# Kernel tuning notes

Hardware: AMD Instinct MI355X
Metric: run time of the kernel (lower is better)

The kernel has to match this reference:

```python
import jax, jax.numpy as jnp
import numpy as np

DIM = 1024
NE = 4            # num_experts
MLP = 4           # mlp_ratio
H = 16            # num_heads
HD = DIM // H     # head dim
EXP = 3 * DIM + MLP * DIM   # expand output dim (7*dim)
CIN = DIM + MLP * DIM       # contract input dim (5*dim)


def layer_norm(x, g, b, eps=1e-5):
    m = jnp.mean(x, axis=-1, keepdims=True)
    v = jnp.var(x, axis=-1, keepdims=True)
    return (x - m) * jax.lax.rsqrt(v + eps) * g + b


def setup_inputs() -> dict:
    key = jax.random.key(0)
    ks = jax.random.split(key, 8)
    B, N = 8, 1024
    x = jax.random.normal(ks[0], (B, N, DIM), jnp.float32)
    expert_mask = jax.random.randint(ks[1], (B, N), 0, NE, jnp.int32)
    router_probs = jax.random.uniform(ks[2], (B, N, NE), jnp.float32)
    expand_weight = jax.random.normal(ks[3], (EXP, DIM), jnp.float32) * 0.02
    mlp_bias = jnp.zeros((MLP * DIM,), jnp.float32)
    contract_weight = jax.random.normal(ks[4], (2 * DIM, CIN), jnp.float32) * 0.02
    contract_bias = jnp.zeros((2 * DIM,), jnp.float32)
    norm1_g = jnp.ones((DIM,), jnp.float32)
    norm1_b = jnp.zeros((DIM,), jnp.float32)
    norm2_g = jnp.ones((DIM,), jnp.float32)
    norm2_b = jnp.zeros((DIM,), jnp.float32)
    alpha = jnp.zeros((1,), jnp.float32)
    return dict(x=x, expert_mask=expert_mask, router_probs=router_probs,
                expand_weight=expand_weight, mlp_bias=mlp_bias,
                contract_weight=contract_weight, contract_bias=contract_bias,
                norm1_g=norm1_g, norm1_b=norm1_b, norm2_g=norm2_g, norm2_b=norm2_b,
                alpha=alpha)


def reference(x, expert_mask, router_probs, expand_weight, mlp_bias,
              contract_weight, contract_bias, norm1_g, norm1_b,
              norm2_g, norm2_b, alpha):
    B, N, _ = x.shape
    shift = (NE - 1 - expert_mask).astype(jnp.int32)          # [B,N]
    # nested (matryoshka) active dims per token
    d_in = DIM // jnp.left_shift(1, shift)                    # expand: active input dims
    d_out = (2 * DIM) // jnp.left_shift(1, shift)             # contract: active output dims

    # nested_linear_expand: zero inactive input features, then full GEMM
    in_mask = (jnp.arange(DIM) < d_in[..., None]).astype(x.dtype)
    xn = layer_norm(x, norm1_g, norm1_b) * in_mask
    y = jnp.einsum('bnd,od->bno', xn, expand_weight)          # [B,N,7*dim]

    qkv = y[..., :3 * DIM]
    mlp_hidden = y[..., 3 * DIM:] + mlp_bias

    q = qkv[..., :DIM]
    k = layer_norm(qkv[..., DIM:2 * DIM], norm2_g, norm2_b)
    v = layer_norm(qkv[..., 2 * DIM:], norm2_g, norm2_b)

    qh = q.reshape(B, N, H, HD)
    kh = k.reshape(B, N, H, HD)
    vh = v.reshape(B, N, H, HD)
    scale = HD ** -0.5
    attn = jax.nn.softmax(jnp.einsum('bqhd,bkhd->bhqk', qh, kh) * scale, axis=-1)
    attn_out = jnp.einsum('bhqk,bkhd->bqhd', attn, vh).reshape(B, N, DIM)

    h = jnp.concatenate([attn_out, jax.nn.gelu(mlp_hidden, approximate=False)], axis=-1)
    # nested_linear_contract: full GEMM, zero inactive output features
    z = jnp.einsum('bnc,oc->bno', h, contract_weight) + contract_bias  # [B,N,2*dim]
    z = z * (jnp.arange(2 * DIM) < d_out[..., None]).astype(z.dtype)

    attn_o = z[..., :DIM] + x
    mlp_o = z[..., DIM:]
    expert_probs = jnp.take_along_axis(router_probs, expert_mask[..., None].astype(jnp.int32), axis=-1)  # [B,N,1]
    out = attn_o + (alpha * expert_probs + 1.0) * mlp_o
    return (out, expert_mask, router_probs)
```

## Files before the change

kernel.cpp:

```cpp
#include <hip/hip_runtime.h>
#include <hip/hip_bf16.h>
#include <math.h>

typedef __bf16 bf16_t;
typedef __attribute__((ext_vector_type(8))) __bf16 bf16x8;
typedef __attribute__((ext_vector_type(4))) __bf16 bf16x4;
typedef __attribute__((ext_vector_type(4))) float f32x4;
typedef __attribute__((ext_vector_type(4))) unsigned u32x4;

typedef __attribute__((address_space(1))) unsigned as1u;
typedef __attribute__((address_space(3))) unsigned as3u;

#define MAXT1 68
#define MAXJ2 2112

__device__ __forceinline__ void async_copy16(bf16_t* lds, const bf16_t* g) {
  __builtin_amdgcn_global_load_lds((as1u*)g, (as3u*)lds, 16, 0, 0);
}

__device__ __forceinline__ float gelu_exact(float t) {
  return 0.5f * t * (1.0f + erff(t * 0.70710678118654752f));
}

__device__ __forceinline__ unsigned pack_bf16(float a, float b) {
  unsigned short ha = __builtin_bit_cast(unsigned short, (bf16_t)a);
  unsigned short hb = __builtin_bit_cast(unsigned short, (bf16_t)b);
  return (unsigned)ha | ((unsigned)hb << 16);
}

__global__ __launch_bounds__(256)
void cast_kernel(const float* __restrict__ w, bf16_t* __restrict__ o, int n) {
  int i = (blockIdx.x * 256 + threadIdx.x) * 4;
  if (i < n) {
    float4 v = *(const float4*)(w + i);
    bf16x4 t;
    t[0] = (bf16_t)v.x; t[1] = (bf16_t)v.y; t[2] = (bf16_t)v.z; t[3] = (bf16_t)v.w;
    *(bf16x4*)(o + i) = t;
  }
}

__global__ __launch_bounds__(1024)
void sort_kernel(const int* __restrict__ em, int* __restrict__ perm,
                 int* __restrict__ t1, int* __restrict__ j2) {
  __shared__ int cnt[4], cur[4], tb[5], jb[5];
  const int tid = threadIdx.x;
  const int wave = tid >> 6, lane = tid & 63;
  if (tid < 4) cnt[tid] = 0;
  __syncthreads();
  for (int c = wave; c < 128; c += 16) {
    int e = em[c * 64 + lane];
    unsigned long long m0 = __ballot(e == 0), m1 = __ballot(e == 1);
    unsigned long long m2 = __ballot(e == 2), m3 = __ballot(e == 3);
    if (lane == 0) {
      atomicAdd(&cnt[0], (int)__popcll(m0)); atomicAdd(&cnt[1], (int)__popcll(m1));
      atomicAdd(&cnt[2], (int)__popcll(m2)); atomicAdd(&cnt[3], (int)__popcll(m3));
    }
  }
  __syncthreads();
  if (tid == 0) {
    cur[0] = 0; cur[1] = cnt[0]; cur[2] = cnt[0] + cnt[1]; cur[3] = cnt[0] + cnt[1] + cnt[2];
    tb[0] = 0; jb[0] = 0;
    for (int i = 0; i < 4; ++i) {
      int e = 3 - i;
      tb[i + 1] = tb[i] + ((cnt[e] + 127) >> 7);
    }
    for (int e = 0; e < 4; ++e) {
      int nt = (cnt[e] + 127) >> 7;
      jb[e + 1] = jb[e] + nt * (4 << e);
    }
  }
  __syncthreads();
  for (int c = wave; c < 128; c += 16) {
    int i = c * 64 + lane;
    int e = em[i];
    unsigned long long m0 = __ballot(e == 0), m1 = __ballot(e == 1);
    unsigned long long m2 = __ballot(e == 2), m3 = __ballot(e == 3);
    unsigned long long me = e == 0 ? m0 : e == 1 ? m1 : e == 2 ? m2 : m3;
    int bl = 0;
    if (lane < 4) {
      unsigned long long ml = lane == 0 ? m0 : lane == 1 ? m1 : lane == 2 ? m2 : m3;
      bl = atomicAdd(&cur[lane], (int)__popcll(ml));
    }
    int base = __shfl(bl, e);
    unsigned long long lt = (1ull << lane) - 1ull;
    perm[base + (int)__popcll(me & lt)] = i;
  }
  int offp[5];
  offp[0] = 0;
  #pragma unroll
  for (int e = 0; e < 4; ++e) offp[e + 1] = offp[e] + cnt[e];
  for (int t = tid; t < MAXT1; t += 1024) {
    int e = -1, loc = 0;
    #pragma unroll
    for (int i = 0; i < 4; ++i) if (t >= tb[i] && t < tb[i + 1]) { e = 3 - i; loc = t - tb[i]; }
    if (e >= 0) {
      t1[t * 3] = e; t1[t * 3 + 1] = offp[e] + loc * 128;
      t1[t * 3 + 2] = min(128, cnt[e] - loc * 128);
    } else t1[t * 3] = -1;
  }
  for (int j = tid; j < MAXJ2; j += 1024) {
    int e = -1, loc = 0;
    #pragma unroll
    for (int q = 0; q < 4; ++q) if (j >= jb[q] && j < jb[q + 1]) { e = q; loc = j - jb[q]; }
    if (e >= 0) {
      int t = loc >> (2 + e), b = loc & ((4 << e) - 1);
      j2[j * 4] = e; j2[j * 4 + 1] = offp[e] + t * 128;
      j2[j * 4 + 2] = min(128, cnt[e] - t * 128); j2[j * 4 + 3] = b;
    } else j2[j * 4] = -1;
  }
}

__global__ __launch_bounds__(256)
void ln1_kernel(const float* __restrict__ x, const float* __restrict__ gam,
                const float* __restrict__ bet, const int* __restrict__ em,
                bf16_t* __restrict__ xn) {
  const int row = blockIdx.x, tid = threadIdx.x;
  const float4 v = ((const float4*)(x + (size_t)row * 1024))[tid];
  float s = v.x + v.y + v.z + v.w;
  float sq = v.x * v.x + v.y * v.y + v.z * v.z + v.w * v.w;
  #pragma unroll
  for (int off = 1; off < 64; off <<= 1) { s += __shfl_xor(s, off); sq += __shfl_xor(sq, off); }
  __shared__ float red[8];
  const int wave = tid >> 6, lane = tid & 63;
  if (lane == 0) { red[wave] = s; red[4 + wave] = sq; }
  __syncthreads();
  s = red[0] + red[1] + red[2] + red[3];
  sq = red[4] + red[5] + red[6] + red[7];
  const float mean = s * (1.0f / 1024.0f);
  const float var = sq * (1.0f / 1024.0f) - mean * mean;
  const float rstd = rsqrtf(var + 1e-5f);
  const int din = 1024 >> (3 - em[row]);
  const float4 gv = ((const float4*)gam)[tid];
  const float4 bv = ((const float4*)bet)[tid];
  const int c0 = tid * 4;
  float vf[4] = {v.x, v.y, v.z, v.w};
  float gf[4] = {gv.x, gv.y, gv.z, gv.w};
  float bvf[4] = {bv.x, bv.y, bv.z, bv.w};
  bf16x4 o;
  #pragma unroll
  for (int i = 0; i < 4; ++i) {
    float t = (vf[i] - mean) * rstd * gf[i] + bvf[i];
    o[i] = (c0 + i < din) ? (bf16_t)t : (bf16_t)0.0f;
  }
  *(bf16x4*)(xn + (size_t)row * 1024 + c0) = o;
}

__global__ __launch_bounds__(256)
void ln2_kernel(bf16_t* __restrict__ kv, const float* __restrict__ gam,
                const float* __restrict__ bet) {
  const int row = blockIdx.x, tid = threadIdx.x;
  bf16_t* base = kv + (size_t)row * 2048;
  bf16x4 kk = *(const bf16x4*)(base + tid * 4);
  bf16x4 vv = *(const bf16x4*)(base + 1024 + tid * 4);
  float kf[4], vf[4];
  float ks = 0, ksq = 0, vs = 0, vsq = 0;
  #pragma unroll
  for (int i = 0; i < 4; ++i) {
    kf[i] = (float)kk[i]; ks += kf[i]; ksq += kf[i] * kf[i];
    vf[i] = (float)vv[i]; vs += vf[i]; vsq += vf[i] * vf[i];
  }
  #pragma unroll
  for (int off = 1; off < 64; off <<= 1) {
    ks += __shfl_xor(ks, off); ksq += __shfl_xor(ksq, off);
    vs += __shfl_xor(vs, off); vsq += __shfl_xor(vsq, off);
  }
  __shared__ float red[16];
  const int wave = tid >> 6, lane = tid & 63;
  if (lane == 0) { red[wave] = ks; red[4 + wave] = ksq; red[8 + wave] = vs; red[12 + wave] = vsq; }
  __syncthreads();
  ks = red[0] + red[1] + red[2] + red[3];
  ksq = red[4] + red[5] + red[6] + red[7];
  vs = red[8] + red[9] + red[10] + red[11];
  vsq = red[12] + red[13] + red[14] + red[15];
  const float mk = ks * (1.f / 1024.f), mv = vs * (1.f / 1024.f);
  const float rk = rsqrtf(ksq * (1.f / 1024.f) - mk * mk + 1e-5f);
  const float rv = rsqrtf(vsq * (1.f / 1024.f) - mv * mv + 1e-5f);
  const float4 gv = ((const float4*)gam)[tid];
  const float4 bv = ((const float4*)bet)[tid];
  float gf[4] = {gv.x, gv.y, gv.z, gv.w}, bvf[4] = {bv.x, bv.y, bv.z, bv.w};
  bf16x4 ko, vo;
  #pragma unroll
  for (int i = 0; i < 4; ++i) {
    ko[i] = (bf16_t)((kf[i] - mk) * rk * gf[i] + bvf[i]);
    vo[i] = (bf16_t)((vf[i] - mv) * rv * gf[i] + bvf[i]);
  }
  *(bf16x4*)(base + tid * 4) = ko;
  *(bf16x4*)(base + 1024 + tid * 4) = vo;
}

__global__ __launch_bounds__(256)
void vt_kernel(const bf16_t* __restrict__ kv, bf16_t* __restrict__ vT) {
  __shared__ bf16_t t[64][80];
  const int tt = blockIdx.x, head = blockIdx.y;
  const int tid = threadIdx.x;
  const int r8 = tid >> 3, c8 = tid & 7;
  #pragma unroll
  for (int i = 0; i < 2; ++i) {
    const int tok = i * 32 + r8;
    bf16x8 v = *(const bf16x8*)(kv + (size_t)(tt * 64 + tok) * 2048 + 1024 + head * 64 + c8 * 8);
    #pragma unroll
    for (int j = 0; j < 8; ++j) t[c8 * 8 + j][tok] = v[j];
  }
  __syncthreads();
  const int bb = tt >> 4;
  const int tloc = (tt & 15) * 64;
  #pragma unroll
  for (int i = 0; i < 2; ++i) {
    const int d = i * 32 + r8;
    bf16x8 v = *(const bf16x8*)(&t[d][c8 * 8]);
    *(bf16x8*)(vT + (size_t)((bb * 16 + head) * 64 + d) * 1024 + tloc + c8 * 8) = v;
  }
}

template<int EPI>
__global__ __launch_bounds__(256)
void gemm_bt(const bf16_t* __restrict__ A, const bf16_t* __restrict__ W,
             const int* __restrict__ perm, const int* __restrict__ desc,
             const float* __restrict__ bias,
             bf16_t* __restrict__ hb, bf16_t* __restrict__ kvb,
             bf16_t* __restrict__ z) {
  constexpr int K = (EPI == 0) ? 1024 : 5120;
  constexpr int BN = (EPI == 0) ? 128 : 64;
  constexpr int NI = BN / 32;
  constexpr int WC = BN / 2;
  const int* d = desc + ((EPI == 0) ? blockIdx.y * 3 : blockIdx.x * 4);
  const int e = d[0];
  if (e < 0) return;
  const int nval = d[2];
  const int bn = (EPI == 0) ? blockIdx.x : d[3];
  const int nkt = (EPI == 0) ? (2 << e) : 80;

  __shared__ bf16_t SMEM[17408];
  __shared__ int prow[128];
  bf16_t* As = SMEM;
  bf16_t* Bs = SMEM + 8192;

  const int tid = threadIdx.x;
  if (tid < 128) prow[tid] = perm[d[1] + min(tid, nval - 1)];
  const int wave = tid >> 6, lane = tid & 63;
  const int l15 = lane & 15, l4 = lane >> 4;
  const int wm = wave >> 1, wn = wave & 1;

  f32x4 acc[4][NI] = {};

  const int rbase = tid >> 3;
  const int ss = (tid & 7) ^ (rbase & 7);
  __syncthreads();
  const bf16_t* Ag[4];
  #pragma unroll
  for (int i = 0; i < 4; ++i) Ag[i] = A + (size_t)prow[i * 32 + rbase] * K + ss * 8;
  const bf16_t* Wg = W + (size_t)(bn * BN + rbase) * K + ss * 8;

  for (int kt = 0; kt < nkt; ++kt) {
    #pragma unroll
    for (int i = 0; i < 4; ++i)
      async_copy16(As + (i * 256 + wave * 64) * 8, Ag[i] + kt * 64);
    #pragma unroll
    for (int i = 0; i < NI; ++i)
      async_copy16(Bs + (i * 256 + wave * 64) * 8, Wg + (size_t)(i * 32) * K + kt * 64);
    __syncthreads();
    #pragma unroll
    for (int ks = 0; ks < 2; ++ks) {
      bf16x8 a[4], b[NI];
      #pragma unroll
      for (int mi = 0; mi < 4; ++mi) {
        const int r = wm * 64 + mi * 16 + l15;
        const int slot = (ks * 4 + l4) ^ (r & 7);
        a[mi] = *(const bf16x8*)(As + r * 64 + slot * 8);
      }
      #pragma unroll
      for (int ni = 0; ni < NI; ++ni) {
        const int r = wn * WC + ni * 16 + l15;
        const int slot = (ks * 4 + l4) ^ (r & 7);
        b[ni] = *(const bf16x8*)(Bs + r * 64 + slot * 8);
      }
      #pragma unroll
      for (int mi = 0; mi < 4; ++mi)
        #pragma unroll
        for (int ni = 0; ni < NI; ++ni)
          acc[mi][ni] = __builtin_amdgcn_mfma_f32_16x16x32_bf16(a[mi], b[ni], acc[mi][ni], 0, 0, 0);
    }
    __syncthreads();
  }

  #pragma unroll
  for (int mi = 0; mi < 4; ++mi) {
    #pragma unroll
    for (int ni = 0; ni < NI; ++ni) {
      const int colf = wn * WC + ni * 16 + l15;
      #pragma unroll
      for (int r = 0; r < 4; ++r) {
        const int row = wm * 64 + mi * 16 + l4 * 4 + r;
        const float c = acc[mi][ni][r];
        bf16_t v;
        if (EPI == 0) {
          const int gc = bn * 128 + colf;
          v = (gc >= 3072) ? (bf16_t)gelu_exact(c + bias[gc - 3072]) : (bf16_t)c;
        } else {
          v = (bf16_t)(c + bias[bn * 64 + colf]);
        }
        SMEM[row * 136 + colf] = v;
      }
    }
  }
  __syncthreads();
  if (EPI == 0) {
    const int col0 = (tid & 15) * 8;
    const int gc0 = bn * 128 + col0;
    #pragma unroll
    for (int i = 0; i < 8; ++i) {
      const int row = (tid >> 4) * 8 + i;
      if (row < nval) {
        const size_t token = (size_t)prow[row];
        bf16x8 v = *(const bf16x8*)(SMEM + row * 136 + col0);
        if (gc0 < 1024)      *(bf16x8*)(hb + token * 5120 + gc0) = v;
        else if (gc0 < 3072) *(bf16x8*)(kvb + token * 2048 + (gc0 - 1024)) = v;
        else                 *(bf16x8*)(hb + token * 5120 + 1024 + (gc0 - 3072)) = v;
      }
    }
  } else {
    const int col0 = (tid & 7) * 8;
    const int gc0 = bn * 64 + col0;
    #pragma unroll
    for (int i = 0; i < 4; ++i) {
      const int row = (tid >> 3) * 4 + i;
      if (row < nval) {
        const size_t token = (size_t)prow[row];
        bf16x8 v = *(const bf16x8*)(SMEM + row * 136 + col0);
        *(bf16x8*)(z + token * 2048 + gc0) = v;
      }
    }
  }
}

__global__ __launch_bounds__(256)
void attn_kernel(const bf16_t* __restrict__ kv, const bf16_t* __restrict__ vT,
                 bf16_t* __restrict__ hb) {
  __shared__ bf16_t Kl[64 * 64];
  __shared__ bf16_t Vl[64 * 64];
  const int tid = threadIdx.x;
  const int wave = tid >> 6, lane = tid & 63;
  const int l15 = lane & 15, l4 = lane >> 4;
  const int qt = blockIdx.x, bh = blockIdx.y;
  const int bb = bh >> 4;
  const int tok0 = bb << 10;
  const int d0 = (bh & 15) << 6;

  const int qrow = tok0 + qt * 64 + wave * 16 + l15;
  const bf16x8 bq0 = *(const bf16x8*)(hb + (size_t)qrow * 5120 + d0 + l4 * 8);
  const bf16x8 bq1 = *(const bf16x8*)(hb + (size_t)qrow * 5120 + d0 + 32 + l4 * 8);

  f32x4 o[4] = {};
  float mrun = -1e30f, lrun = 0.f;

  const int krb = tid >> 3;
  const int kss = (tid & 7) ^ (krb & 7);
  const int idx0 = ((2 * (l4 & 1) + 0) * 16 + l15) * 4;
  const int idx1 = ((2 * (l4 & 1) + 1) * 16 + l15) * 4;
  const bool hi = (l4 >> 1) != 0;

  for (int kt = 0; kt < 16; ++kt) {
    const int krow0 = tok0 + kt * 64;
    #pragma unroll
    for (int i = 0; i < 2; ++i) {
      async_copy16(Kl + (i * 256 + wave * 64) * 8,
                   kv + (size_t)(krow0 + i * 32 + krb) * 2048 + d0 + kss * 8);
      async_copy16(Vl + (i * 256 + wave * 64) * 8,
                   vT + (size_t)(bh * 64 + i * 32 + krb) * 1024 + kt * 64 + kss * 8);
    }
    __syncthreads();

    f32x4 s[4] = {};
    #pragma unroll
    for (int ks = 0; ks < 2; ++ks) {
      const bf16x8 bq = ks ? bq1 : bq0;
      #pragma unroll
      for (int kc = 0; kc < 4; ++kc) {
        const int r = kc * 16 + l15;
        const int slot = (ks * 4 + l4) ^ (r & 7);
        bf16x8 ak = *(const bf16x8*)(Kl + r * 64 + slot * 8);
        s[kc] = __builtin_amdgcn_mfma_f32_16x16x32_bf16(ak, bq, s[kc], 0, 0, 0);
      }
    }

    float mx = s[0][0];
    #pragma unroll
    for (int kc = 0; kc < 4; ++kc)
      #pragma unroll
      for (int r = 0; r < 4; ++r) mx = fmaxf(mx, s[kc][r]);
    mx = fmaxf(mx, __shfl_xor(mx, 16));
    mx = fmaxf(mx, __shfl_xor(mx, 32));
    mx *= 0.125f;
    const float mnew = fmaxf(mrun, mx);
    const float corr = __expf(mrun - mnew);
    float ps = 0.f;
    #pragma unroll
    for (int kc = 0; kc < 4; ++kc)
      #pragma unroll
      for (int r = 0; r < 4; ++r) {
        const float p = __expf(s[kc][r] * 0.125f - mnew);
        s[kc][r] = p;
        ps += p;
      }
    ps += __shfl_xor(ps, 16);
    ps += __shfl_xor(ps, 32);
    lrun = lrun * corr + ps;
    mrun = mnew;

    unsigned pd[4][2], bp[4][2][2];
    #pragma unroll
    for (int kc = 0; kc < 4; ++kc) {
      pd[kc][0] = pack_bf16(s[kc][0], s[kc][1]);
      pd[kc][1] = pack_bf16(s[kc][2], s[kc][3]);
    }
    #pragma unroll
    for (int kc = 0; kc < 4; ++kc)
      #pragma unroll
      for (int rp = 0; rp < 2; ++rp) {
        bp[kc][rp][0] = (unsigned)__builtin_amdgcn_ds_bpermute(idx0, (int)pd[kc][rp]);
        bp[kc][rp][1] = (unsigned)__builtin_amdgcn_ds_bpermute(idx1, (int)pd[kc][rp]);
      }
    u32x4 w0, w1;
    w0[0] = hi ? bp[1][0][0] : bp[0][0][0];
    w0[1] = hi ? bp[1][1][0] : bp[0][1][0];
    w0[2] = hi ? bp[1][0][1] : bp[0][0][1];
    w0[3] = hi ? bp[1][1][1] : bp[0][1][1];
    w1[0] = hi ? bp[3][0][0] : bp[2][0][0];
    w1[1] = hi ? bp[3][1][0] : bp[2][1][0];
    w1[2] = hi ? bp[3][0][1] : bp[2][0][1];
    w1[3] = hi ? bp[3][1][1] : bp[2][1][1];
    const bf16x8 pa0 = __builtin_bit_cast(bf16x8, w0);
    const bf16x8 pa1 = __builtin_bit_cast(bf16x8, w1);

    float cq[4];
    #pragma unroll
    for (int r = 0; r < 4; ++r) cq[r] = __shfl(corr, l4 * 4 + r);
    #pragma unroll
    for (int dn = 0; dn < 4; ++dn)
      #pragma unroll
      for (int r = 0; r < 4; ++r) o[dn][r] *= cq[r];

    #pragma unroll
    for (int dn = 0; dn < 4; ++dn) {
      const int r = dn * 16 + l15;
      bf16x8 bv0 = *(const bf16x8*)(Vl + r * 64 + ((l4 ^ (r & 7)) * 8));
      bf16x8 bv1 = *(const bf16x8*)(Vl + r * 64 + (((4 + l4) ^ (r & 7)) * 8));
      o[dn] = __builtin_amdgcn_mfma_f32_16x16x32_bf16(pa0, bv0, o[dn], 0, 0, 0);
      o[dn] = __builtin_amdgcn_mfma_f32_16x16x32_bf16(pa1, bv1, o[dn], 0, 0, 0);
    }
    __syncthreads();
  }

  const float il = 1.0f / lrun;
  float linv[4];
  #pragma unroll
  for (int r = 0; r < 4; ++r) linv[r] = __shfl(il, l4 * 4 + r);
  #pragma unroll
  for (int r = 0; r < 4; ++r) {
    const int gq = tok0 + qt * 64 + wave * 16 + l4 * 4 + r;
    #pragma unroll
    for (int dn = 0; dn < 4; ++dn)
      hb[(size_t)gq * 5120 + d0 + dn * 16 + l15] = (bf16_t)(o[dn][r] * linv[r]);
  }
}

__global__ __launch_bounds__(256)
void final_kernel(const bf16_t* __restrict__ z, const float* __restrict__ x,
                  const int* __restrict__ em, const float* __restrict__ rp,
                  const float* __restrict__ alpha, float* __restrict__ out) {
  const int row = blockIdx.x, tid = threadIdx.x;
  const int e = em[row];
  const int dout = 2048 >> (3 - e);
  const float f = alpha[0] * rp[row * 4 + e] + 1.0f;
  const bf16x4 z0 = ((const bf16x4*)(z + (size_t)row * 2048))[tid];
  const bf16x4 z1 = ((const bf16x4*)(z + (size_t)row * 2048 + 1024))[tid];
  const float4 xv = ((const float4*)(x + (size_t)row * 1024))[tid];
  const int c = tid * 4;
  float4 o;
  o.x = ((c + 0) < dout ? (float)z0[0] : 0.f) + xv.x + f * ((1024 + c + 0) < dout ? (float)z1[0] : 0.f);
  o.y = ((c + 1) < dout ? (float)z0[1] : 0.f) + xv.y + f * ((1024 + c + 1) < dout ? (float)z1[1] : 0.f);
  o.z = ((c + 2) < dout ? (float)z0[2] : 0.f) + xv.z + f * ((1024 + c + 2) < dout ? (float)z1[2] : 0.f);
  o.w = ((c + 3) < dout ? (float)z0[3] : 0.f) + xv.w + f * ((1024 + c + 3) < dout ? (float)z1[3] : 0.f);
  ((float4*)(out + (size_t)row * 1024))[tid] = o;
  float* out_em = out + 8388608;
  float* out_rp = out_em + 8192;
  if (tid == 0) out_em[row] = (float)e;
  if (tid < 4) out_rp[row * 4 + tid] = rp[row * 4 + tid];
}

extern "C" void kernel_launch(void* const* d_in, const int* in_sizes, int n_in,
                              void* d_out, int out_size, void* d_ws, size_t ws_size,
                              hipStream_t stream) {
  const float* x = (const float*)d_in[0];
  const int* em = (const int*)d_in[1];
  const float* rp = (const float*)d_in[2];
  const float* w_exp = (const float*)d_in[3];
  const float* mlp_bias = (const float*)d_in[4];
  const float* w_con = (const float*)d_in[5];
  const float* c_bias = (const float*)d_in[6];
  const float* n1g = (const float*)d_in[7];
  const float* n1b = (const float*)d_in[8];
  const float* n2g = (const float*)d_in[9];
  const float* n2b = (const float*)d_in[10];
  const float* alpha = (const float*)d_in[11];

  char* ws = (char*)d_ws;
  bf16_t* Wexp = (bf16_t*)ws;
  bf16_t* xn   = (bf16_t*)(ws + 14680064);
  bf16_t* vT   = (bf16_t*)(ws + 14680064);
  int*    perm = (int*)(ws + 31457280);
  int*    t1d  = (int*)(ws + 31457280 + 32768);
  int*    j2d  = (int*)(ws + 31457280 + 34816);
  bf16_t* kvb  = (bf16_t*)(ws + 48234496);
  bf16_t* z    = (bf16_t*)(ws + 48234496);
  bf16_t* Wcon = (bf16_t*)(ws + 81788928);
  bf16_t* hb   = (bf16_t*)(ws + 102760448);

  sort_kernel<<<1, 1024, 0, stream>>>(em, perm, t1d, j2d);
  cast_kernel<<<7168, 256, 0, stream>>>(w_exp, Wexp, 7340032);
  cast_kernel<<<10240, 256, 0, stream>>>(w_con, Wcon, 10485760);
  ln1_kernel<<<8192, 256, 0, stream>>>(x, n1g, n1b, em, xn);
  gemm_bt<0><<<dim3(56, MAXT1), 256, 0, stream>>>(xn, Wexp, perm, t1d, mlp_bias,
                                                  hb, kvb, nullptr);
  ln2_kernel<<<8192, 256, 0, stream>>>(kvb, n2g, n2b);
  vt_kernel<<<dim3(128, 16), 256, 0, stream>>>(kvb, vT);
  attn_kernel<<<dim3(16, 128), 256, 0, stream>>>(kvb, vT, hb);
  gemm_bt<1><<<MAXJ2, 256, 0, stream>>>(hb, Wcon, perm, j2d, c_bias,
                                        nullptr, nullptr, z);
  final_kernel<<<8192, 256, 0, stream>>>(z, x, em, rp, alpha, (float*)d_out);
}
```

Before: 439.4 us.

## Shrink GEMM LDS footprint, drop prow staging, reorder tile schedule, add MFMA priority

The tile schedule for the expand and contract GEMMs now orders the contract jobs by expert from largest to smallest, matching the expand ordering. The GEMM kernel no longer stages permuted row indices in shared memory. Each thread reads perm directly, which removes one barrier. The expand epilogue is split into two 64-column halves so the LDS buffer shrinks, aiming for higher occupancy, at the cost of extra barriers and repeated perm loads. The attention kernel also raises wave priority around its MFMA sections.

```diff
diff --git a/kernel.cpp b/kernel.cpp
--- a/kernel.cpp
+++ b/kernel.cpp
@@ -62,11 +62,9 @@
     tb[0] = 0; jb[0] = 0;
     for (int i = 0; i < 4; ++i) {
       int e = 3 - i;
-      tb[i + 1] = tb[i] + ((cnt[e] + 127) >> 7);
-    }
-    for (int e = 0; e < 4; ++e) {
       int nt = (cnt[e] + 127) >> 7;
-      jb[e + 1] = jb[e] + nt * (4 << e);
+      tb[i + 1] = tb[i] + nt;
+      jb[i + 1] = jb[i] + nt * (4 << e);
     }
   }
   __syncthreads();
@@ -101,7 +99,7 @@
   for (int j = tid; j < MAXJ2; j += 1024) {
     int e = -1, loc = 0;
     #pragma unroll
-    for (int q = 0; q < 4; ++q) if (j >= jb[q] && j < jb[q + 1]) { e = q; loc = j - jb[q]; }
+    for (int i = 0; i < 4; ++i) if (j >= jb[i] && j < jb[i + 1]) { e = 3 - i; loc = j - jb[i]; }
     if (e >= 0) {
       int t = loc >> (2 + e), b = loc & ((4 << e) - 1);
       j2[j * 4] = e; j2[j * 4 + 1] = offp[e] + t * 128;
@@ -226,17 +224,16 @@
   const int* d = desc + ((EPI == 0) ? blockIdx.y * 3 : blockIdx.x * 4);
   const int e = d[0];
   if (e < 0) return;
+  const int d1 = d[1];
   const int nval = d[2];
   const int bn = (EPI == 0) ? blockIdx.x : d[3];
   const int nkt = (EPI == 0) ? (2 << e) : 80;
 
-  __shared__ bf16_t SMEM[17408];
-  __shared__ int prow[128];
+  __shared__ bf16_t SMEM[(EPI == 0) ? 16384 : 12288];
   bf16_t* As = SMEM;
   bf16_t* Bs = SMEM + 8192;
 
   const int tid = threadIdx.x;
-  if (tid < 128) prow[tid] = perm[d[1] + min(tid, nval - 1)];
   const int wave = tid >> 6, lane = tid & 63;
   const int l15 = lane & 15, l4 = lane >> 4;
   const int wm = wave >> 1, wn = wave & 1;
@@ -245,10 +242,12 @@
 
   const int rbase = tid >> 3;
   const int ss = (tid & 7) ^ (rbase & 7);
-  __syncthreads();
   const bf16_t* Ag[4];
   #pragma unroll
-  for (int i = 0; i < 4; ++i) Ag[i] = A + (size_t)prow[i * 32 + rbase] * K + ss * 8;
+  for (int i = 0; i < 4; ++i) {
+    const int pr = perm[d1 + min(i * 32 + rbase, nval - 1)];
+    Ag[i] = A + (size_t)pr * K + ss * 8;
+  }
   const bf16_t* Wg = W + (size_t)(bn * BN + rbase) * K + ss * 8;
 
   for (int kt = 0; kt < nkt; ++kt) {
@@ -283,51 +282,64 @@
     __syncthreads();
   }
 
-  #pragma unroll
-  for (int mi = 0; mi < 4; ++mi) {
-    #pragma unroll
-    for (int ni = 0; ni < NI; ++ni) {
-      const int colf = wn * WC + ni * 16 + l15;
-      #pragma unroll
-      for (int r = 0; r < 4; ++r) {
-        const int row = wm * 64 + mi * 16 + l4 * 4 + r;
-        const float c = acc[mi][ni][r];
-        bf16_t v;
-        if (EPI == 0) {
-          const int gc = bn * 128 + colf;
-          v = (gc >= 3072) ? (bf16_t)gelu_exact(c + bias[gc - 3072]) : (bf16_t)c;
-        } else {
-          v = (bf16_t)(c + bias[bn * 64 + colf]);
+  if (EPI == 0) {
+    #pragma unroll
+    for (int half = 0; half < 2; ++half) {
+      if (wn == half) {
+        #pragma unroll
+        for (int mi = 0; mi < 4; ++mi) {
+          #pragma unroll
+          for (int ni = 0; ni < NI; ++ni) {
+            const int colf = ni * 16 + l15;
+            const int gc = bn * 128 + half * 64 + colf;
+            #pragma unroll
+            for (int r = 0; r < 4; ++r) {
+              const int row = wm * 64 + mi * 16 + l4 * 4 + r;
+              const float c = acc[mi][ni][r];
+              SMEM[row * 72 + colf] =
+                  (gc >= 3072) ? (bf16_t)gelu_exact(c + bias[gc - 3072]) : (bf16_t)c;
+            }
+          }
         }
-        SMEM[row * 136 + colf] = v;
-      }
-    }
-  }
-  __syncthreads();
-  if (EPI == 0) {
-    const int col0 = (tid & 15) * 8;
-    const int gc0 = bn * 128 + col0;
-    #pragma unroll
-    for (int i = 0; i < 8; ++i) {
-      const int row = (tid >> 4) * 8 + i;
-      if (row < nval) {
-        const size_t token = (size_t)prow[row];
-        bf16x8 v = *(const bf16x8*)(SMEM + row * 136 + col0);
-        if (gc0 < 1024)      *(bf16x8*)(hb + token * 5120 + gc0) = v;
-        else if (gc0 < 3072) *(bf16x8*)(kvb + token * 2048 + (gc0 - 1024)) = v;
-        else                 *(bf16x8*)(hb + token * 5120 + 1024 + (gc0 - 3072)) = v;
-      }
+      }
+      __syncthreads();
+      const int col0 = (tid & 7) * 8;
+      const int gc0 = bn * 128 + half * 64 + col0;
+      #pragma unroll
+      for (int i = 0; i < 4; ++i) {
+        const int row = (tid >> 3) * 4 + i;
+        if (row < nval) {
+          const size_t token = (size_t)perm[d1 + row];
+          bf16x8 v = *(const bf16x8*)(SMEM + row * 72 + col0);
+          if (gc0 < 1024)      *(bf16x8*)(hb + token * 5120 + gc0) = v;
+          else if (gc0 < 3072) *(bf16x8*)(kvb + token * 2048 + (gc0 - 1024)) = v;
+          else                 *(bf16x8*)(hb + token * 5120 + 1024 + (gc0 - 3072)) = v;
+        }
+      }
+      __syncthreads();
     }
   } else {
+    #pragma unroll
+    for (int mi = 0; mi < 4; ++mi) {
+      #pragma unroll
+      for (int ni = 0; ni < NI; ++ni) {
+        const int colf = wn * WC + ni * 16 + l15;
+        #pragma unroll
+        for (int r = 0; r < 4; ++r) {
+          const int row = wm * 64 + mi * 16 + l4 * 4 + r;
+          SMEM[row * 72 + colf] = (bf16_t)(acc[mi][ni][r] + bias[bn * 64 + colf]);
+        }
+      }
+    }
+    __syncthreads();
     const int col0 = (tid & 7) * 8;
-    const int gc0 = bn * 64 + col0;
     #pragma unroll
     for (int i = 0; i < 4; ++i) {
       const int row = (tid >> 3) * 4 + i;
       if (row < nval) {
-        const size_t token = (size_t)prow[row];
-        bf16x8 v = *(const bf16x8*)(SMEM + row * 136 + col0);
-        *(bf16x8*)(z + token * 2048 + gc0) = v;
+        const size_t token = (size_t)perm[d1 + row];
+        bf16x8 v = *(const bf16x8*)(SMEM + row * 72 + col0);
+        *(bf16x8*)(z + token * 2048 + bn * 64 + col0) = v;
       }
     }
   }
@@ -371,6 +383,7 @@
     __syncthreads();
 
     f32x4 s[4] = {};
+    __builtin_amdgcn_s_setprio(1);
     #pragma unroll
     for (int ks = 0; ks < 2; ++ks) {
       const bf16x8 bq = ks ? bq1 : bq0;
@@ -382,6 +395,7 @@
         s[kc] = __builtin_amdgcn_mfma_f32_16x16x32_bf16(ak, bq, s[kc], 0, 0, 0);
       }
     }
+    __builtin_amdgcn_s_setprio(0);
 
     float mx = s[0][0];
     #pragma unroll
@@ -440,6 +454,7 @@
       #pragma unroll
       for (int r = 0; r < 4; ++r) o[dn][r] *= cq[r];
 
+    __builtin_amdgcn_s_setprio(1);
     #pragma unroll
     for (int dn = 0; dn < 4; ++dn) {
       const int r = dn * 16 + l15;
@@ -448,6 +463,7 @@
       o[dn] = __builtin_amdgcn_mfma_f32_16x16x32_bf16(pa0, bv0, o[dn], 0, 0, 0);
       o[dn] = __builtin_amdgcn_mfma_f32_16x16x32_bf16(pa1, bv1, o[dn], 0, 0, 0);
     }
+    __builtin_amdgcn_s_setprio(0);
     __syncthreads();
   }
 
```

Result: slower. 468.7 us (+6.7%).
